# Kernel optimization log

Hardware: AMD Instinct MI355X
Metric: run time of the kernel (lower is better)

The kernel has to match this reference:

```python
import jax, jax.numpy as jnp
import numpy as np

TILE = 128  # hardcoded tile size in tile_cache/untile_cache


def setup_inputs() -> dict:
    key = jax.random.key(0)
    k1, k2 = jax.random.split(key)
    B, H, D, T = 4, 8, 128, 64  # max_len = TILE * T = 8192
    # K stored tiled-transposed: (B, H, D, 128, num_tiles)
    k_cache = jax.random.normal(k1, (B, H, D, TILE, T), dtype=jnp.float32)
    # V stored tiled: (B, H, 128, num_tiles, D)
    v_cache = jax.random.normal(k2, (B, H, TILE, T, D), dtype=jnp.float32)
    return {"k_cache": k_cache, "v_cache": v_cache, "seq_len": 6144}


def reference(k_cache, v_cache, seq_len):
    # untile_cache, transposed=True: (B,H,D,128,T) -> (B,H,D,128*T)  [BHDS]
    B, H, D, tile, T = k_cache.shape
    k = k_cache.reshape(B, H, D, tile * T)
    # untile_cache, transposed=False: (B,H,128,T,D) -> (B,H,128*T,D)  [BHSD]
    Bv, Hv, tile_v, Tv, Dv = v_cache.shape
    v = v_cache.reshape(Bv, Hv, tile_v * Tv, Dv)
    # _slice_kv_cacheline, padding_side='right': slice [0, seq_len) on seq dim
    k = k[:, :, :, :seq_len]        # seq dim = 3 (transposed K)
    v = v[:, :, :seq_len, :]        # seq dim = 2
    # stack into a single output: transpose K back to BHSD to match V layout
    k_bhsd = jnp.swapaxes(k, 2, 3)  # (B,H,S,D)
    return jnp.stack([k_bhsd, v], axis=0)  # (2, B, H, seq_len, D)
```

## Files before the change

### kernel.cpp

```cpp
#include <hip/hip_runtime.h>


#define BH 32
#define DD 128

__global__ __launch_bounds__(256) void kv_repack(
    const float* __restrict__ kc, const float* __restrict__ vc,
    float* __restrict__ out,
    int S, int Sfull, int kBlocks, int vBlocksPerBH, int f4PerVBlock)
{
    const int bid = blockIdx.x;
    if (bid < kBlocks) {
        const int sTilesPerBH = S >> 7;
        const int bh    = bid / sTilesPerBH;
        const int sTile = bid - bh * sTilesPerBH;
        const int t     = threadIdx.x;
        const int lane  = t & 63;
        const int wave  = t >> 6;
        const int dhalf = wave & 1;
        const int ssub  = wave >> 1;
        const int d     = (dhalf << 6) + lane;
        const int s0    = (sTile << 7) + (ssub << 6);

        const float* src = kc + (size_t)(bh * DD + d) * (size_t)Sfull + s0;
        float* dst = out + ((size_t)bh * S + s0) * DD + (dhalf << 6) + lane;

#pragma unroll
        for (int j = 0; j < 16; ++j) {
            float4 v4 = *(const float4*)(src + (j << 2));
            float* drow = dst + (size_t)(j << 2) * DD;
            drow[0]       = v4.x;
            drow[DD]      = v4.y;
            drow[2 * DD]  = v4.z;
            drow[3 * DD]  = v4.w;
        }
    } else {
        const int vb   = bid - kBlocks;
        const int bh   = vb / vBlocksPerBH;
        const int part = vb - bh * vBlocksPerBH;

        const size_t f4PerBHsrc = (size_t)Sfull * (DD / 4);
        const size_t f4PerBHdst = (size_t)S * (DD / 4);
        const size_t outVOff    = (size_t)BH * S * (DD / 4);

        const float4* src = (const float4*)vc + (size_t)bh * f4PerBHsrc
                            + (size_t)part * f4PerVBlock;
        float4* dst = (float4*)out + outVOff + (size_t)bh * f4PerBHdst
                      + (size_t)part * f4PerVBlock;

        for (int i = threadIdx.x; i < f4PerVBlock; i += 256)
            dst[i] = src[i];
    }
}

extern "C" void kernel_launch(void* const* d_in, const int* in_sizes, int n_in,
                              void* d_out, int out_size, void* d_ws, size_t ws_size,
                              hipStream_t stream) {
    const float* kc = (const float*)d_in[0];
    const float* vc = (const float*)d_in[1];
    float* out = (float*)d_out;

    const int S     = out_size / (2 * BH * DD);
    const int Sfull = in_sizes[0] / (BH * DD);

    const int kBlocks       = BH * (S >> 7);
    const int vBlocksPerBH  = S >> 7;
    const int f4PerVBlock   = (S * (DD / 4)) / vBlocksPerBH;
    const int vBlocks       = BH * vBlocksPerBH;

    dim3 grid(kBlocks + vBlocks);
    dim3 block(256);
    kv_repack<<<grid, block, 0, stream>>>(kc, vc, out, S, Sfull,
                                          kBlocks, vBlocksPerBH, f4PerVBlock);
}
```

Before: 364.6 us.

## Transpose K tiles through padded LDS for coalesced float4 stores

The K transpose now stages a 64x128 tile in shared memory, padded to avoid bank conflicts. Reads are coalesced float4 loads along the sequence dimension and writes are coalesced float4 stores along D, where before each lane wrote scattered scalars. The K work is split across twice as many blocks, each handling half of D. This adds an LDS round trip and a barrier, and raises per-block shared memory use, which also applies to the V-copy blocks.

Result: faster. 357.3 us (-2.0%).

```diff
diff --git a/kernel.cpp b/kernel.cpp
--- a/kernel.cpp
+++ b/kernel.cpp
@@ -3,36 +3,58 @@
 
 #define BH 32
 #define DD 128
+#define LDS_STRIDE 129
 
 __global__ __launch_bounds__(256) void kv_repack(
     const float* __restrict__ kc, const float* __restrict__ vc,
     float* __restrict__ out,
     int S, int Sfull, int kBlocks, int vBlocksPerBH, int f4PerVBlock)
 {
+    __shared__ float lds[64 * LDS_STRIDE];
+
     const int bid = blockIdx.x;
+    const int t = threadIdx.x;
+
     if (bid < kBlocks) {
-        const int sTilesPerBH = S >> 7;
-        const int bh    = bid / sTilesPerBH;
-        const int sTile = bid - bh * sTilesPerBH;
-        const int t     = threadIdx.x;
-        const int lane  = t & 63;
-        const int wave  = t >> 6;
-        const int dhalf = wave & 1;
-        const int ssub  = wave >> 1;
-        const int d     = (dhalf << 6) + lane;
-        const int s0    = (sTile << 7) + (ssub << 6);
+        const int sTiles = S >> 7;
+        const int perBH  = 2 * sTiles;
+        const int bh     = bid / perBH;
+        const int rem    = bid - bh * perBH;
+        const int dTile  = rem / sTiles;
+        const int sTile  = rem - dTile * sTiles;
 
-        const float* src = kc + (size_t)(bh * DD + d) * (size_t)Sfull + s0;
-        float* dst = out + ((size_t)bh * S + s0) * DD + (dhalf << 6) + lane;
+        {
+            const int s4 = t & 31;
+            const int d0 = t >> 5;
+            const float* src = kc
+                + (size_t)(bh * DD + dTile * 64) * (size_t)Sfull
+                + (size_t)(sTile << 7) + (s4 << 2);
+#pragma unroll
+            for (int i = 0; i < 8; ++i) {
+                const int d = d0 + (i << 3);
+                float4 v = *(const float4*)(src + (size_t)d * Sfull);
+                float* L = &lds[d * LDS_STRIDE + (s4 << 2)];
+                L[0] = v.x; L[1] = v.y; L[2] = v.z; L[3] = v.w;
+            }
+        }
+        __syncthreads();
 
+        {
+            const int d4 = t & 15;
+            const int r0 = t >> 4;
+            float* dstBase = out
+                + ((size_t)bh * S + (size_t)(sTile << 7)) * DD
+                + dTile * 64 + (d4 << 2);
 #pragma unroll
-        for (int j = 0; j < 16; ++j) {
-            float4 v4 = *(const float4*)(src + (j << 2));
-            float* drow = dst + (size_t)(j << 2) * DD;
-            drow[0]       = v4.x;
-            drow[DD]      = v4.y;
-            drow[2 * DD]  = v4.z;
-            drow[3 * DD]  = v4.w;
+            for (int i = 0; i < 8; ++i) {
+                const int sr = (i << 4) + r0;
+                float4 v;
+                v.x = lds[(4 * d4 + 0) * LDS_STRIDE + sr];
+                v.y = lds[(4 * d4 + 1) * LDS_STRIDE + sr];
+                v.z = lds[(4 * d4 + 2) * LDS_STRIDE + sr];
+                v.w = lds[(4 * d4 + 3) * LDS_STRIDE + sr];
+                *(float4*)(dstBase + (size_t)sr * DD) = v;
+            }
         }
     } else {
         const int vb   = bid - kBlocks;
@@ -48,7 +70,7 @@
         float4* dst = (float4*)out + outVOff + (size_t)bh * f4PerBHdst
                       + (size_t)part * f4PerVBlock;
 
-        for (int i = threadIdx.x; i < f4PerVBlock; i += 256)
+        for (int i = t; i < f4PerVBlock; i += 256)
             dst[i] = src[i];
     }
 }
@@ -63,8 +85,9 @@
     const int S     = out_size / (2 * BH * DD);
     const int Sfull = in_sizes[0] / (BH * DD);
 
-    const int kBlocks       = BH * (S >> 7);
-    const int vBlocksPerBH  = S >> 7;
+    const int sTiles        = S >> 7;
+    const int kBlocks       = BH * 2 * sTiles;
+    const int vBlocksPerBH  = sTiles;
     const int f4PerVBlock   = (S * (DD / 4)) / vBlocksPerBH;
     const int vBlocks       = BH * vBlocksPerBH;
 
```
